# Optimization experiments

Hardware: AMD Instinct MI355X
Metric: run time of the kernel (lower is better)

## Reference

```python
import jax, jax.numpy as jnp
import numpy as np

NUM_USERS = 200000
NUM_ITEMS = 100000
N_NODES = NUM_USERS + NUM_ITEMS
NNZ = 4000000
LATENT_DIM = 64
N_LAYERS = 3


def setup_inputs() -> dict:
    key = jax.random.key(0)
    k1, k2, k3, k4, k5 = jax.random.split(key, 5)
    user_emb = jax.random.normal(k1, (NUM_USERS, LATENT_DIM), dtype=jnp.float32) * 0.1
    item_emb = jax.random.normal(k2, (NUM_ITEMS, LATENT_DIM), dtype=jnp.float32) * 0.1
    vals = jax.random.uniform(k3, (NNZ,), dtype=jnp.float32)
    rows = jax.random.randint(k4, (NNZ,), 0, N_NODES)
    cols = jax.random.randint(k5, (NNZ,), 0, N_NODES)
    return {"user_emb": user_emb, "item_emb": item_emb, "vals": vals,
            "rows": rows, "cols": cols}


def _spmm(vals, rows, cols, x):
    # y[r] += vals[e] * x[cols[e]]  -- COO SpMM, equivalent to torch.sparse.mm
    msgs = vals[:, None] * x[cols]          # [nnz, d]
    return jax.ops.segment_sum(msgs, rows, num_segments=N_NODES)


def reference(user_emb, item_emb, vals, rows, cols):
    # LightGCN.computer(), eval path: L = ones, no dropout, norm_emb=False
    all_emb = jnp.concatenate([user_emb, item_emb], axis=0)  # [N, d]
    emb = all_emb
    acc = all_emb
    for _ in range(N_LAYERS):
        emb = _spmm(vals, rows, cols, emb)
        acc = acc + emb
    light_out = acc / jnp.asarray(N_LAYERS + 1, dtype=acc.dtype)  # mean over layers
    users = light_out[:NUM_USERS]
    items = light_out[NUM_USERS:]
    return users, items
```

## Files before the change

kernel.cpp:

```cpp
#include <hip/hip_runtime.h>

#define NUM_USERS 200000
#define NUM_ITEMS 100000
#define N_NODES   300000
#define NNZ       4000000
#define DIM       64
#define N_ELEM   ((size_t)N_NODES * DIM)

#define BKT_SHIFT 6
#define NBKT      ((N_NODES + 63) >> 6)
#define NSUB      8
#define PAD       32

static __device__ __forceinline__ float bf2f(unsigned short v) {
    return __uint_as_float(((unsigned int)v) << 16);
}
static __device__ __forceinline__ unsigned short f2bf(float f) {
    unsigned int u = __float_as_uint(f);
    u = (u + 0x7FFF + ((u >> 16) & 1)) >> 16;
    return (unsigned short)u;
}

__global__ void lgcn_convert(const float4* __restrict__ user4,
                             const float4* __restrict__ item4,
                             ushort4* __restrict__ bufC) {
    size_t i = (size_t)blockIdx.x * blockDim.x + threadIdx.x;
    const size_t n4 = N_ELEM / 4, nu4 = (size_t)NUM_USERS * DIM / 4;
    if (i >= n4) return;
    float4 v = (i < nu4) ? user4[i] : item4[i - nu4];
    ushort4 o;
    o.x = f2bf(v.x); o.y = f2bf(v.y); o.z = f2bf(v.z); o.w = f2bf(v.w);
    bufC[i] = o;
}

__global__ void lgcn_bhist(const int4* __restrict__ rows4, int* __restrict__ bcnt) {
    int i = blockIdx.x * blockDim.x + threadIdx.x;
    if (i >= NNZ / 4) return;
    int g = (i >> 6) & (NSUB - 1);
    int4 r = rows4[i];
    atomicAdd(&bcnt[(((r.x >> BKT_SHIFT) << 3) + g) * PAD], 1);
    atomicAdd(&bcnt[(((r.y >> BKT_SHIFT) << 3) + g) * PAD], 1);
    atomicAdd(&bcnt[(((r.z >> BKT_SHIFT) << 3) + g) * PAD], 1);
    atomicAdd(&bcnt[(((r.w >> BKT_SHIFT) << 3) + g) * PAD], 1);
}

__global__ void lgcn_balloc(const int* __restrict__ bcnt, int* __restrict__ bbase,
                            int* __restrict__ btot, int* __restrict__ bfill,
                            int* __restrict__ cursor) {
    int b = blockIdx.x * blockDim.x + threadIdx.x;
    int lane = threadIdx.x & 63;
    int cg[NSUB];
    int tot = 0;
    if (b < NBKT) {
        #pragma unroll
        for (int g = 0; g < NSUB; ++g) {
            cg[g] = bcnt[((b << 3) + g) * PAD];
            tot += cg[g];
        }
    }
    int s = tot;
    #pragma unroll
    for (int o = 1; o < 64; o <<= 1) {
        int t = __shfl_up(s, o);
        if (lane >= o) s += t;
    }
    int wtot = __shfl(s, 63);
    int wbase = 0;
    if (lane == 63) wbase = atomicAdd(cursor, wtot);
    wbase = __shfl(wbase, 63);
    if (b < NBKT) {
        int base = wbase + (s - tot);
        bbase[b] = base;
        btot[b]  = tot;
        int run = base;
        #pragma unroll
        for (int g = 0; g < NSUB; ++g) {
            bfill[((b << 3) + g) * PAD] = run;
            run += cg[g];
        }
    }
}

__global__ void lgcn_append(const int* __restrict__ rows, const int* __restrict__ cols,
                            const float* __restrict__ vals, int* __restrict__ bfill,
                            int2* __restrict__ staging) {
    int e = blockIdx.x * blockDim.x + threadIdx.x;
    if (e >= NNZ) return;
    int g = blockIdx.x & (NSUB - 1);
    int r = rows[e];
    int b = r >> BKT_SHIFT;
    int p = atomicAdd(&bfill[((b << 3) + g) * PAD], 1);
    staging[p] = make_int2(((r & 63) << 19) | cols[e], __float_as_int(vals[e]));
}

__global__ __launch_bounds__(256) void lgcn_bsort(
    const int2* __restrict__ staging, const int* __restrict__ bbase,
    const int* __restrict__ btot, int2* __restrict__ desc, int2* __restrict__ sc)
{
    __shared__ int cnt64[64], fill64[64];
    int b   = blockIdx.x;
    int tid = threadIdx.x;
    if (tid < 64) cnt64[tid] = 0;
    __syncthreads();
    int base = bbase[b];
    int n    = btot[b];

    for (int i = tid; i < n; i += 256)
        atomicAdd(&cnt64[staging[base + i].x >> 19], 1);
    __syncthreads();

    if (tid < 64) {
        int c = cnt64[tid];
        int s = c;
        #pragma unroll
        for (int o = 1; o < 64; o <<= 1) {
            int t = __shfl_up(s, o);
            if (tid >= o) s += t;
        }
        int off = s - c;
        fill64[tid] = off;
        int row = (b << BKT_SHIFT) + tid;
        if (row < N_NODES) desc[row] = make_int2(base + off, c);
    }
    __syncthreads();

    for (int i = tid; i < n; i += 256) {
        int2 e = staging[base + i];
        int lr = e.x >> 19;
        int p = atomicAdd(&fill64[lr], 1);
        sc[base + p] = make_int2(e.x & 0x7FFFF, e.y);
    }
}

template<int MODE>
__global__ __launch_bounds__(256) void lgcn_spmm_csr(
    const int2* __restrict__ desc, const int2* __restrict__ sc,
    const unsigned short* __restrict__ cur, unsigned short* __restrict__ nxt,
    const float* __restrict__ user_emb, const float* __restrict__ item_emb,
    const unsigned short* __restrict__ e1buf, const unsigned short* __restrict__ e2buf,
    float* __restrict__ out)
{
    int row  = blockIdx.x * 4 + (threadIdx.x >> 6);
    int lane = threadIdx.x & 63;
    if (row >= N_NODES) return;
    int2 d = desc[row];
    int b = d.x, n = d.y;
    float acc0 = 0.f, acc1 = 0.f, acc2 = 0.f, acc3 = 0.f;

    for (int k0 = 0; k0 < n; k0 += 64) {
        int m = min(64, n - k0);
        int c = 0, vbits = 0;
        if (lane < m) {
            int2 cv = sc[b + k0 + lane];
            c = cv.x; vbits = cv.y;
        }
        int m8 = (m + 7) & ~7;
        for (int j = 0; j < m8; j += 8) {
            int   cc[8];
            float vv[8];
            #pragma unroll
            for (int t = 0; t < 8; ++t) {
                cc[t] = __shfl(c, j + t);
                vv[t] = __int_as_float(__shfl(vbits, j + t));
            }
            float x[8];
            #pragma unroll
            for (int t = 0; t < 8; ++t)
                x[t] = bf2f(cur[(size_t)cc[t] * DIM + lane]);
            acc0 += vv[0] * x[0];
            acc1 += vv[1] * x[1];
            acc2 += vv[2] * x[2];
            acc3 += vv[3] * x[3];
            acc0 += vv[4] * x[4];
            acc1 += vv[5] * x[5];
            acc2 += vv[6] * x[6];
            acc3 += vv[7] * x[7];
        }
    }

    float acc = (acc0 + acc1) + (acc2 + acc3);
    size_t o = (size_t)row * DIM + lane;
    if constexpr (MODE == 1) {
        nxt[o] = f2bf(acc);
    } else {
        float own = (row < NUM_USERS)
                  ? user_emb[o]
                  : item_emb[(size_t)(row - NUM_USERS) * DIM + lane];
        out[o] = 0.25f * (own + bf2f(e1buf[o]) + bf2f(e2buf[o]) + acc);
    }
}

extern "C" void kernel_launch(void* const* d_in, const int* in_sizes, int n_in,
                              void* d_out, int out_size, void* d_ws, size_t ws_size,
                              hipStream_t stream) {
    const float* user_emb = (const float*)d_in[0];
    const float* item_emb = (const float*)d_in[1];
    const float* vals     = (const float*)d_in[2];
    const int*   rows     = (const int*)d_in[3];
    const int*   cols     = (const int*)d_in[4];
    float* out = (float*)d_out;

    char* ws = (char*)d_ws;
    size_t off = 0;
    unsigned short* bufC = (unsigned short*)(ws + off); off += N_ELEM * 2;
    unsigned short* buf0 = (unsigned short*)(ws + off); off += N_ELEM * 2;
    unsigned short* buf1 = (unsigned short*)(ws + off); off += N_ELEM * 2;
    int2* staging = (int2*)(ws + off); off += (size_t)NNZ * 8;
    int2* sc      = (int2*)(ws + off); off += (size_t)NNZ * 8;
    int2* desc    = (int2*)(ws + off); off += (size_t)N_NODES * 8;
    int*  bcnt    = (int*) (ws + off); off += (size_t)NBKT * NSUB * PAD * 4;
    int*  cursor  = (int*) (ws + off); off += 256;
    int*  bbase   = (int*) (ws + off); off += (size_t)NBKT * 4;
    int*  btot    = (int*) (ws + off); off += (size_t)NBKT * 4;
    int*  bfill   = (int*) (ws + off); off += (size_t)NBKT * NSUB * PAD * 4;

    const int BLK = 256;
    dim3 grid_conv((unsigned)((N_ELEM / 4 + BLK - 1) / BLK));
    dim3 grid_edge((NNZ + BLK - 1) / BLK);
    dim3 grid_edge4((NNZ / 4 + BLK - 1) / BLK);
    dim3 grid_bkt((NBKT + BLK - 1) / BLK);
    dim3 grid_sort(NBKT);
    dim3 grid_spmm((N_NODES + 3) / 4);

    hipMemsetAsync(bcnt, 0, (size_t)NBKT * NSUB * PAD * 4 + 256, stream);
    lgcn_convert<<<grid_conv, BLK, 0, stream>>>(
        (const float4*)user_emb, (const float4*)item_emb, (ushort4*)bufC);
    lgcn_bhist<<<grid_edge4, BLK, 0, stream>>>((const int4*)rows, bcnt);
    lgcn_balloc<<<grid_bkt, BLK, 0, stream>>>(bcnt, bbase, btot, bfill, cursor);
    lgcn_append<<<grid_edge, BLK, 0, stream>>>(rows, cols, vals, bfill, staging);
    lgcn_bsort<<<grid_sort, BLK, 0, stream>>>(staging, bbase, btot, desc, sc);

    lgcn_spmm_csr<1><<<grid_spmm, BLK, 0, stream>>>(
        desc, sc, bufC, buf0, nullptr, nullptr, nullptr, nullptr, nullptr);
    lgcn_spmm_csr<1><<<grid_spmm, BLK, 0, stream>>>(
        desc, sc, buf0, buf1, nullptr, nullptr, nullptr, nullptr, nullptr);
    lgcn_spmm_csr<2><<<grid_spmm, BLK, 0, stream>>>(
        desc, sc, buf1, nullptr, user_emb, item_emb, buf0, buf1, out);
}
```

Measured before the change: 888.1 us.

## Gather two bf16 per lane with half-wave edge split, widen sort buckets

The SpMM gather now has each lane load a 32-bit word holding two bf16 features. The two half-waves each handle alternate edges, and their partial sums are combined with a cross-half shuffle at the end. This doubles the number of edges in flight per load instruction and halves the gather instruction count. Separately, the bucket sort uses 256-row buckets with a shared-memory block scan instead of 64-row buckets with a wave scan. That cuts the number of sort blocks but adds barrier-heavy scan steps.

New measurement: 854.8 us. -3.8%, faster.

```diff
diff --git a/kernel.cpp b/kernel.cpp
--- a/kernel.cpp
+++ b/kernel.cpp
@@ -7,14 +7,14 @@
 #define DIM       64
 #define N_ELEM   ((size_t)N_NODES * DIM)
 
-#define BKT_SHIFT 6
-#define NBKT      ((N_NODES + 63) >> 6)
+#define BKT_SHIFT 8
+#define BKT_ROWS  256
+#define NBKT      ((N_NODES + BKT_ROWS - 1) >> BKT_SHIFT)
 #define NSUB      8
 #define PAD       32
 
-static __device__ __forceinline__ float bf2f(unsigned short v) {
-    return __uint_as_float(((unsigned int)v) << 16);
-}
+typedef unsigned int uint32;
+
 static __device__ __forceinline__ unsigned short f2bf(float f) {
     unsigned int u = __float_as_uint(f);
     u = (u + 0x7FFF + ((u >> 16) & 1)) >> 16;
@@ -90,44 +90,45 @@
     int r = rows[e];
     int b = r >> BKT_SHIFT;
     int p = atomicAdd(&bfill[((b << 3) + g) * PAD], 1);
-    staging[p] = make_int2(((r & 63) << 19) | cols[e], __float_as_int(vals[e]));
+    staging[p] = make_int2(((r & (BKT_ROWS - 1)) << 19) | cols[e],
+                           __float_as_int(vals[e]));
 }
 
 __global__ __launch_bounds__(256) void lgcn_bsort(
     const int2* __restrict__ staging, const int* __restrict__ bbase,
     const int* __restrict__ btot, int2* __restrict__ desc, int2* __restrict__ sc)
 {
-    __shared__ int cnt64[64], fill64[64];
+    __shared__ int cnt[BKT_ROWS], pfx[BKT_ROWS], fill[BKT_ROWS];
     int b   = blockIdx.x;
     int tid = threadIdx.x;
-    if (tid < 64) cnt64[tid] = 0;
+    cnt[tid] = 0;
     __syncthreads();
     int base = bbase[b];
     int n    = btot[b];
 
     for (int i = tid; i < n; i += 256)
-        atomicAdd(&cnt64[staging[base + i].x >> 19], 1);
-    __syncthreads();
-
-    if (tid < 64) {
-        int c = cnt64[tid];
-        int s = c;
-        #pragma unroll
-        for (int o = 1; o < 64; o <<= 1) {
-            int t = __shfl_up(s, o);
-            if (tid >= o) s += t;
-        }
-        int off = s - c;
-        fill64[tid] = off;
-        int row = (b << BKT_SHIFT) + tid;
-        if (row < N_NODES) desc[row] = make_int2(base + off, c);
-    }
+        atomicAdd(&cnt[staging[base + i].x >> 19], 1);
+    __syncthreads();
+
+    int c = cnt[tid];
+    pfx[tid] = c;
+    __syncthreads();
+    for (int o = 1; o < 256; o <<= 1) {
+        int t = (tid >= o) ? pfx[tid - o] : 0;
+        __syncthreads();
+        pfx[tid] += t;
+        __syncthreads();
+    }
+    int excl = pfx[tid] - c;
+    fill[tid] = excl;
+    int row = (b << BKT_SHIFT) + tid;
+    if (row < N_NODES) desc[row] = make_int2(base + excl, c);
     __syncthreads();
 
     for (int i = tid; i < n; i += 256) {
         int2 e = staging[base + i];
         int lr = e.x >> 19;
-        int p = atomicAdd(&fill64[lr], 1);
+        int p = atomicAdd(&fill[lr], 1);
         sc[base + p] = make_int2(e.x & 0x7FFFF, e.y);
     }
 }
@@ -135,17 +136,19 @@
 template<int MODE>
 __global__ __launch_bounds__(256) void lgcn_spmm_csr(
     const int2* __restrict__ desc, const int2* __restrict__ sc,
-    const unsigned short* __restrict__ cur, unsigned short* __restrict__ nxt,
-    const float* __restrict__ user_emb, const float* __restrict__ item_emb,
-    const unsigned short* __restrict__ e1buf, const unsigned short* __restrict__ e2buf,
-    float* __restrict__ out)
+    const uint32* __restrict__ cur2, uint32* __restrict__ nxt2,
+    const float2* __restrict__ user2, const float2* __restrict__ item2,
+    const uint32* __restrict__ e1b, const uint32* __restrict__ e2b,
+    float2* __restrict__ out2)
 {
     int row  = blockIdx.x * 4 + (threadIdx.x >> 6);
     int lane = threadIdx.x & 63;
     if (row >= N_NODES) return;
     int2 d = desc[row];
     int b = d.x, n = d.y;
-    float acc0 = 0.f, acc1 = 0.f, acc2 = 0.f, acc3 = 0.f;
+    int half = lane >> 5;
+    int hl   = lane & 31;
+    float accA_lo = 0.f, accA_hi = 0.f, accB_lo = 0.f, accB_hi = 0.f;
 
     for (int k0 = 0; k0 < n; k0 += 64) {
         int m = min(64, n - k0);
@@ -154,39 +157,50 @@
             int2 cv = sc[b + k0 + lane];
             c = cv.x; vbits = cv.y;
         }
-        int m8 = (m + 7) & ~7;
-        for (int j = 0; j < m8; j += 8) {
-            int   cc[8];
-            float vv[8];
+        int m16 = (m + 15) & ~15;
+        for (int j = 0; j < m16; j += 16) {
+            int    idx[8];
+            float  vv[8];
+            uint32 x[8];
             #pragma unroll
             for (int t = 0; t < 8; ++t) {
-                cc[t] = __shfl(c, j + t);
-                vv[t] = __int_as_float(__shfl(vbits, j + t));
+                int src = j + 2 * t + half;
+                idx[t] = __shfl(c, src);
+                vv[t]  = __int_as_float(__shfl(vbits, src));
             }
-            float x[8];
             #pragma unroll
             for (int t = 0; t < 8; ++t)
-                x[t] = bf2f(cur[(size_t)cc[t] * DIM + lane]);
-            acc0 += vv[0] * x[0];
-            acc1 += vv[1] * x[1];
-            acc2 += vv[2] * x[2];
-            acc3 += vv[3] * x[3];
-            acc0 += vv[4] * x[4];
-            acc1 += vv[5] * x[5];
-            acc2 += vv[6] * x[6];
-            acc3 += vv[7] * x[7];
-        }
-    }
-
-    float acc = (acc0 + acc1) + (acc2 + acc3);
-    size_t o = (size_t)row * DIM + lane;
-    if constexpr (MODE == 1) {
-        nxt[o] = f2bf(acc);
-    } else {
-        float own = (row < NUM_USERS)
-                  ? user_emb[o]
-                  : item_emb[(size_t)(row - NUM_USERS) * DIM + lane];
-        out[o] = 0.25f * (own + bf2f(e1buf[o]) + bf2f(e2buf[o]) + acc);
+                x[t] = cur2[idx[t] * 32 + hl];
+            #pragma unroll
+            for (int t = 0; t < 8; ++t) {
+                float xlo = __uint_as_float(x[t] << 16);
+                float xhi = __uint_as_float(x[t] & 0xFFFF0000u);
+                if (t & 1) { accB_lo += vv[t] * xlo; accB_hi += vv[t] * xhi; }
+                else       { accA_lo += vv[t] * xlo; accA_hi += vv[t] * xhi; }
+            }
+        }
+    }
+
+    float alo = accA_lo + accB_lo;
+    float ahi = accA_hi + accB_hi;
+    alo += __shfl_xor(alo, 32);
+    ahi += __shfl_xor(ahi, 32);
+
+    if (half == 0) {
+        int off = row * 32 + hl;
+        if constexpr (MODE == 1) {
+            nxt2[off] = ((uint32)f2bf(ahi) << 16) | (uint32)f2bf(alo);
+        } else {
+            float2 own = (row < NUM_USERS) ? user2[off]
+                                           : item2[(row - NUM_USERS) * 32 + hl];
+            uint32 e1 = e1b[off], e2 = e2b[off];
+            float2 o;
+            o.x = 0.25f * (own.x + __uint_as_float(e1 << 16)
+                                 + __uint_as_float(e2 << 16) + alo);
+            o.y = 0.25f * (own.y + __uint_as_float(e1 & 0xFFFF0000u)
+                                 + __uint_as_float(e2 & 0xFFFF0000u) + ahi);
+            out2[off] = o;
+        }
     }
 }
 
@@ -231,9 +245,13 @@
     lgcn_bsort<<<grid_sort, BLK, 0, stream>>>(staging, bbase, btot, desc, sc);
 
     lgcn_spmm_csr<1><<<grid_spmm, BLK, 0, stream>>>(
-        desc, sc, bufC, buf0, nullptr, nullptr, nullptr, nullptr, nullptr);
+        desc, sc, (const uint32*)bufC, (uint32*)buf0,
+        nullptr, nullptr, nullptr, nullptr, nullptr);
     lgcn_spmm_csr<1><<<grid_spmm, BLK, 0, stream>>>(
-        desc, sc, buf0, buf1, nullptr, nullptr, nullptr, nullptr, nullptr);
+        desc, sc, (const uint32*)buf0, (uint32*)buf1,
+        nullptr, nullptr, nullptr, nullptr, nullptr);
     lgcn_spmm_csr<2><<<grid_spmm, BLK, 0, stream>>>(
-        desc, sc, buf1, nullptr, user_emb, item_emb, buf0, buf1, out);
-}
+        desc, sc, (const uint32*)buf1, nullptr,
+        (const float2*)user_emb, (const float2*)item_emb,
+        (const uint32*)buf0, (const uint32*)buf1, (float2*)out);
+}
```
